# Kernel tuning notes

Measured on AMD Instinct MI355X. Metric: run time of the kernel, lower is better.

## Reference

```python
import jax, jax.numpy as jnp
import numpy as np

N_NODES = 50000
N_EDGES = 1600000
D = 128  # input_dim == hidden_dim


def glorot(key, shape):
    lim = float(np.sqrt(6.0 / (shape[0] + shape[1])))
    return jax.random.uniform(key, shape, jnp.float32, -lim, lim)


def setup_inputs() -> dict:
    key = jax.random.key(0)
    ks = jax.random.split(key, 10)
    x = jax.random.normal(ks[0], (N_NODES, D), jnp.float32)
    edge_index = jax.random.randint(ks[1], (2, N_EDGES), 0, N_NODES, jnp.int64)
    edge_attr = jax.random.normal(ks[2], (N_EDGES, D), jnp.float32)
    # SAGEConv params per layer: lin_l (W,b), lin_r (W, no bias)
    W1l = glorot(ks[3], (D, D)); b1l = jnp.zeros((D,), jnp.float32)
    W1r = glorot(ks[4], (D, D))
    W2l = glorot(ks[5], (D, D)); b2l = jnp.zeros((D,), jnp.float32)
    W2r = glorot(ks[6], (D, D))
    return {"x": x, "edge_index": edge_index, "edge_attr": edge_attr,
            "W1l": W1l, "b1l": b1l, "W1r": W1r,
            "W2l": W2l, "b2l": b2l, "W2r": W2r}


def sage_layer(z, src, dst, edge_attr, Wl, bl, Wr):
    # message: gather x_j, add edge_attr, relu  -> [E, D]
    msg = jax.nn.relu(z[src] + edge_attr)
    # mean aggregation at destination nodes
    agg = jax.ops.segment_sum(msg, dst, num_segments=N_NODES)
    cnt = jax.ops.segment_sum(jnp.ones((dst.shape[0], 1), z.dtype), dst,
                              num_segments=N_NODES)
    agg = agg / jnp.maximum(cnt, 1.0)
    # lin_l(agg) + lin_r(x) (root weight, no bias on lin_r)
    return agg @ Wl + bl + z @ Wr


def reference(x, edge_index, edge_attr, W1l, b1l, W1r, W2l, b2l, W2r):
    src, dst = edge_index[0], edge_index[1]
    z = sage_layer(x, src, dst, edge_attr, W1l, b1l, W1r)
    z = jax.nn.relu(z)  # activation between layers; dropout=0, normalize='none'
    z = sage_layer(z, src, dst, edge_attr, W2l, b2l, W2r)
    return z
```

## Files before the change

kernel.cpp:

```cpp
#include <hip/hip_runtime.h>

#define D 128

typedef __attribute__((ext_vector_type(8))) short bf16x8;
typedef __attribute__((ext_vector_type(4))) float f32x4;
typedef __attribute__((ext_vector_type(4))) unsigned short u16x4;
typedef __attribute__((ext_vector_type(4))) unsigned char u8x4;

__device__ inline unsigned short f2bf(float f) {
    union { float f; unsigned u; } v; v.f = f;
    unsigned r = v.u + 0x7FFF + ((v.u >> 16) & 1);
    return (unsigned short)(r >> 16);
}
__device__ inline float bf2f(unsigned short h) {
    union { unsigned u; float f; } v; v.u = ((unsigned)h) << 16; return v.f;
}
__device__ inline unsigned char f2fp8(float f) {
    unsigned u = __float_as_uint(f);
    unsigned s = (u >> 31) << 7;
    unsigned r = (u & 0x7fffffffu) + 0x7FFFF + ((u >> 20) & 1);
    int e = (int)(r >> 23) - 127;
    if (e < -6) return (unsigned char)s;
    return (unsigned char)(s | ((unsigned)(e + 7) << 3) | ((r >> 20) & 7));
}
__device__ inline float fp82f(unsigned c) {
    unsigned ef = (c >> 3) & 0xF, m = c & 7, s = c >> 7;
    unsigned nb = (s << 31) | ((ef + 120) << 23) | (m << 20);
    float nv = __uint_as_float(nb);
    float sv = (s ? -0.001953125f : 0.001953125f) * (float)m;
    return ef ? nv : sv;
}


__global__ __launch_bounds__(256) void prep_kernel(const float* __restrict__ x,
                                                   unsigned short* __restrict__ xb, int n4,
                                                   const int* __restrict__ dst,
                                                   int* __restrict__ cnt, int E,
                                                   const float* __restrict__ W1l,
                                                   const float* __restrict__ W1r,
                                                   const float* __restrict__ W2l,
                                                   const float* __restrict__ W2r,
                                                   unsigned short* __restrict__ Wt1,
                                                   unsigned short* __restrict__ Wt2,
                                                   const float* __restrict__ ea,
                                                   unsigned char* __restrict__ eaq, int nea4,
                                                   int CAST_B, int CNT_B, int EAQ_B) {
    int b = blockIdx.x, tid = threadIdx.x;
    if (b < CAST_B) {
        int i = b * 256 + tid;
        if (i < n4) {
            float4 v = reinterpret_cast<const float4*>(x)[i];
            ushort4 r;
            r.x = f2bf(v.x); r.y = f2bf(v.y); r.z = f2bf(v.z); r.w = f2bf(v.w);
            reinterpret_cast<ushort4*>(xb)[i] = r;
        }
    } else if (b < CAST_B + CNT_B) {
        int e = (b - CAST_B) * 256 + tid;
        if (e < E) atomicAdd(&cnt[dst[e]], 1);
    } else if (b < CAST_B + CNT_B + 128) {
        int c = b - CAST_B - CNT_B;
        int k = tid;
        float v1 = (k < 128) ? W1l[k * 128 + c] : W1r[(k - 128) * 128 + c];
        float v2 = (k < 128) ? W2l[k * 128 + c] : W2r[(k - 128) * 128 + c];
        Wt1[c * 256 + k] = f2bf(v1);
        Wt2[c * 256 + k] = f2bf(v2);
    } else {
        int i0 = (b - CAST_B - CNT_B - 128) * 256 + tid;
        int step = EAQ_B * 256;
        for (int i = i0; i < nea4; i += step) {
            f32x4 v = __builtin_nontemporal_load(
                reinterpret_cast<const f32x4*>(ea) + i);
            u8x4 q;
            q[0] = f2fp8(v[0]); q[1] = f2fp8(v[1]);
            q[2] = f2fp8(v[2]); q[3] = f2fp8(v[3]);
            reinterpret_cast<u8x4*>(eaq)[i] = q;
        }
    }
}


__global__ __launch_bounds__(256) void psum_kernel(const int* __restrict__ cnt,
                                                   int* __restrict__ bsum, int n) {
    __shared__ int wsh[4];
    int b = blockIdx.x, tid = threadIdx.x;
    int i0 = b * 1024 + tid * 4;
    int s = 0;
    #pragma unroll
    for (int j = 0; j < 4; ++j) { int i = i0 + j; if (i < n) s += cnt[i]; }
    #pragma unroll
    for (int d = 1; d < 64; d <<= 1) s += __shfl_xor(s, d, 64);
    if ((tid & 63) == 0) wsh[tid >> 6] = s;
    __syncthreads();
    if (tid == 0) bsum[b] = wsh[0] + wsh[1] + wsh[2] + wsh[3];
}

__global__ __launch_bounds__(256) void fscan_kernel(const int* __restrict__ cnt,
                                                    const int* __restrict__ bsum,
                                                    int* __restrict__ off,
                                                    int* __restrict__ cursor, int n) {
    __shared__ int wsum[4];
    int b = blockIdx.x, tid = threadIdx.x;
    int lane = tid & 63, wv = tid >> 6;
    int bp = 0;
    for (int j = 0; j < b; ++j) bp += bsum[j];
    int i0 = b * 1024 + tid * 4;
    int v[4]; int s = 0;
    #pragma unroll
    for (int j = 0; j < 4; ++j) { int i = i0 + j; v[j] = (i < n) ? cnt[i] : 0; s += v[j]; }
    int sc = s;
    #pragma unroll
    for (int d = 1; d < 64; d <<= 1) { int u = __shfl_up(sc, d, 64); if (lane >= d) sc += u; }
    if (lane == 63) wsum[wv] = sc;
    __syncthreads();
    int wp = 0;
    for (int j = 0; j < wv; ++j) wp += wsum[j];
    int base = bp + wp + sc - s;
    #pragma unroll
    for (int j = 0; j < 4; ++j) {
        int i = i0 + j;
        if (i < n) { cursor[i] = base; off[i + 1] = base + v[j]; }
        base += v[j];
    }
    if (b == 0 && tid == 0) off[0] = 0;
}


__global__ __launch_bounds__(256) void fill_kernel(const int* __restrict__ src,
                                                   const int* __restrict__ dst,
                                                   int* __restrict__ cursor,
                                                   long long* __restrict__ pairs, int E) {
    int e = blockIdx.x * 256 + threadIdx.x;
    if (e < E) {
        int d = dst[e];
        int slot = atomicAdd(&cursor[d], 1);
        pairs[slot] = (long long)(unsigned)src[e] | ((long long)e << 32);
    }
}


__global__ __launch_bounds__(256) void aggregate_kernel(const unsigned short* __restrict__ featb,
                                                        const unsigned char* __restrict__ eaq,
                                                        const int* __restrict__ off,
                                                        const long long* __restrict__ pairs,
                                                        unsigned short* __restrict__ aggb,
                                                        int N) {
    int nd = blockIdx.x * 4 + (threadIdx.x >> 6);
    if (nd >= N) return;
    int t = threadIdx.x & 63;
    int half = t >> 5, l32 = t & 31;
    int s = off[nd], e = off[nd + 1];
    float a0 = 0.f, a1 = 0.f, a2 = 0.f, a3 = 0.f;

    for (int b = s; b < e; b += 64) {
        int cnt = min(64, e - b);
        long long prl = (b + t < e) ? pairs[b + t] : 0LL;
        int psrc = (int)prl;
        int peid = (int)(prl >> 32);

        auto fetch = [&](int idx, f32x4& ev, u16x4& xv) {
            int sidx = __shfl(psrc, idx, 64);
            int eidx = __shfl(peid, idx, 64);
            u8x4 eq = *reinterpret_cast<const u8x4*>(&eaq[(size_t)eidx * D + l32 * 4]);
            ev[0] = fp82f(eq[0]); ev[1] = fp82f(eq[1]);
            ev[2] = fp82f(eq[2]); ev[3] = fp82f(eq[3]);
            xv = *reinterpret_cast<const u16x4*>(&featb[(size_t)sidx * D + l32 * 4]);
        };
        auto accum = [&](const f32x4& ev, const u16x4& xv) {
            a0 += fmaxf(bf2f(xv[0]) + ev[0], 0.f);
            a1 += fmaxf(bf2f(xv[1]) + ev[1], 0.f);
            a2 += fmaxf(bf2f(xv[2]) + ev[2], 0.f);
            a3 += fmaxf(bf2f(xv[3]) + ev[3], 0.f);
        };

        int p = 0;
        for (; p + 8 <= cnt; p += 8) {
            f32x4 e0, e1, e2, e3; u16x4 x0, x1, x2, x3;
            fetch(p + half, e0, x0);
            fetch(p + 2 + half, e1, x1);
            fetch(p + 4 + half, e2, x2);
            fetch(p + 6 + half, e3, x3);
            accum(e0, x0); accum(e1, x1); accum(e2, x2); accum(e3, x3);
        }
        if (p + 4 <= cnt) {
            f32x4 e0, e1; u16x4 x0, x1;
            fetch(p + half, e0, x0);
            fetch(p + 2 + half, e1, x1);
            accum(e0, x0); accum(e1, x1);
            p += 4;
        }
        if (p + 2 <= cnt) {
            f32x4 e0; u16x4 x0;
            fetch(p + half, e0, x0);
            accum(e0, x0);
            p += 2;
        }
        if (p < cnt) {
            f32x4 e0; u16x4 x0;
            fetch(p, e0, x0);
            if (half == 0) accum(e0, x0);
        }
    }

    a0 += __shfl_xor(a0, 32, 64);
    a1 += __shfl_xor(a1, 32, 64);
    a2 += __shfl_xor(a2, 32, 64);
    a3 += __shfl_xor(a3, 32, 64);
    int deg = e - s;
    float inv = 1.f / (float)(deg > 0 ? deg : 1);
    if (half == 0) {
        u16x4 r;
        r[0] = f2bf(a0 * inv); r[1] = f2bf(a1 * inv);
        r[2] = f2bf(a2 * inv); r[3] = f2bf(a3 * inv);
        *reinterpret_cast<u16x4*>(&aggb[(size_t)nd * D + l32 * 4]) = r;
    }
}


template <int RELU, int OUT_BF16>
__global__ __launch_bounds__(256) void gemm_mfma_kernel(const unsigned short* __restrict__ A1,
                                                        const unsigned short* __restrict__ A2,
                                                        const unsigned short* __restrict__ Wt,
                                                        const float* __restrict__ bias,
                                                        float* __restrict__ outf,
                                                        unsigned short* __restrict__ outb,
                                                        int MT, int N) {
    int tid = threadIdx.x;
    int w = tid >> 6;
    int l = tid & 63;
    int lr = l & 15;
    int lg = l >> 4;
    int c0 = w * 32;

    bf16x8 bfr[2][8];
    #pragma unroll
    for (int t = 0; t < 2; ++t)
        #pragma unroll
        for (int kc = 0; kc < 8; ++kc)
            bfr[t][kc] = *reinterpret_cast<const bf16x8*>(
                &Wt[(size_t)(c0 + t * 16 + lr) * 256 + kc * 32 + lg * 8]);

    for (int mt = blockIdx.x; mt < MT; mt += gridDim.x) {
        int r0 = mt * 32;
        f32x4 acc[2][2];
        #pragma unroll
        for (int tr = 0; tr < 2; ++tr)
            #pragma unroll
            for (int tc = 0; tc < 2; ++tc) acc[tr][tc] = {0.f, 0.f, 0.f, 0.f};

        #pragma unroll
        for (int kc = 0; kc < 8; ++kc) {
            const unsigned short* Ap = (kc < 4) ? A1 : A2;
            int k = (kc & 3) * 32 + lg * 8;
            bf16x8 af0 = *reinterpret_cast<const bf16x8*>(&Ap[(size_t)(r0 + lr) * D + k]);
            bf16x8 af1 = *reinterpret_cast<const bf16x8*>(&Ap[(size_t)(r0 + 16 + lr) * D + k]);
            acc[0][0] = __builtin_amdgcn_mfma_f32_16x16x32_bf16(af0, bfr[0][kc], acc[0][0], 0, 0, 0);
            acc[1][0] = __builtin_amdgcn_mfma_f32_16x16x32_bf16(af1, bfr[0][kc], acc[1][0], 0, 0, 0);
            acc[0][1] = __builtin_amdgcn_mfma_f32_16x16x32_bf16(af0, bfr[1][kc], acc[0][1], 0, 0, 0);
            acc[1][1] = __builtin_amdgcn_mfma_f32_16x16x32_bf16(af1, bfr[1][kc], acc[1][1], 0, 0, 0);
        }

        #pragma unroll
        for (int tc = 0; tc < 2; ++tc) {
            int col = c0 + tc * 16 + lr;
            float bv = bias[col];
            #pragma unroll
            for (int tr = 0; tr < 2; ++tr) {
                #pragma unroll
                for (int r = 0; r < 4; ++r) {
                    int row = r0 + tr * 16 + lg * 4 + r;
                    if (row < N) {
                        float v = acc[tr][tc][r] + bv;
                        if (RELU) v = fmaxf(v, 0.f);
                        if (OUT_BF16) outb[(size_t)row * D + col] = f2bf(v);
                        else outf[(size_t)row * D + col] = v;
                    }
                }
            }
        }
    }
}

extern "C" void kernel_launch(void* const* d_in, const int* in_sizes, int n_in,
                              void* d_out, int out_size, void* d_ws, size_t ws_size,
                              hipStream_t stream) {
    const float* x   = (const float*)d_in[0];
    const int*   ei  = (const int*)d_in[1];
    const float* ea  = (const float*)d_in[2];
    const float* W1l = (const float*)d_in[3];
    const float* b1l = (const float*)d_in[4];
    const float* W1r = (const float*)d_in[5];
    const float* W2l = (const float*)d_in[6];
    const float* b2l = (const float*)d_in[7];
    const float* W2r = (const float*)d_in[8];
    float* out = (float*)d_out;

    const int N = in_sizes[0] / D;
    const int E = in_sizes[1] / 2;
    const int NP = (N + 31) & ~31;
    const int* src = ei;
    const int* dst = ei + E;

    char* ws = (char*)d_ws;
    size_t o = 0;
    auto alloc = [&](size_t bytes) -> void* {
        void* p = ws + o;
        o = (o + bytes + 255) & ~(size_t)255;
        return p;
    };
    int*   cnt    = (int*)alloc((size_t)N * 4);
    int*   off    = (int*)alloc((size_t)(N + 1) * 4);
    int*   cursor = (int*)alloc((size_t)N * 4);
    int*   bsum   = (int*)alloc(256 * 4);
    long long* pairs = (long long*)alloc((size_t)E * 8);
    unsigned char* eaq = (unsigned char*)alloc((size_t)E * D);
    unsigned short* xb   = (unsigned short*)alloc((size_t)NP * D * 2);
    unsigned short* z1b  = (unsigned short*)alloc((size_t)NP * D * 2);
    unsigned short* aggb = (unsigned short*)alloc((size_t)NP * D * 2);
    unsigned short* Wt1  = (unsigned short*)alloc(128 * 256 * 2);
    unsigned short* Wt2  = (unsigned short*)alloc(128 * 256 * 2);
    (void)ws_size; (void)n_in; (void)out_size;

    const int MT = (N + 31) / 32;
    const int NB = (N + 1023) / 1024;
    const int AGB = (N + 3) / 4;
    const int n4 = N * D / 4;
    const int nea4 = (int)((size_t)E * D / 4);
    const int CAST_B = (n4 + 255) / 256;
    const int CNT_B = (E + 255) / 256;
    const int EAQ_B = 8192;

    (void)hipMemsetAsync(cnt, 0, (size_t)N * 4, stream);
    prep_kernel<<<CAST_B + CNT_B + 128 + EAQ_B, 256, 0, stream>>>(
        x, xb, n4, dst, cnt, E, W1l, W1r, W2l, W2r, Wt1, Wt2,
        ea, eaq, nea4, CAST_B, CNT_B, EAQ_B);
    psum_kernel<<<NB, 256, 0, stream>>>(cnt, bsum, N);
    fscan_kernel<<<NB, 256, 0, stream>>>(cnt, bsum, off, cursor, N);
    fill_kernel<<<(E + 255) / 256, 256, 0, stream>>>(src, dst, cursor, pairs, E);

    aggregate_kernel<<<AGB, 256, 0, stream>>>(xb, eaq, off, pairs, aggb, N);
    gemm_mfma_kernel<1, 1><<<1024, 256, 0, stream>>>(aggb, xb, Wt1, b1l, nullptr, z1b, MT, N);

    aggregate_kernel<<<AGB, 256, 0, stream>>>(z1b, eaq, off, pairs, aggb, N);
    gemm_mfma_kernel<0, 0><<<1024, 256, 0, stream>>>(aggb, z1b, Wt2, b2l, out, nullptr, MT, N);
}
```

Baseline: 679.1 us.

## Fuse all stages into one cooperative persistent kernel and drop fp8 edge attributes

Replaces the sequence of prep, scan, fill, aggregate and GEMM launches with a single cooperative kernel that runs each stage in turn, separated by grid-wide syncs and using grid-stride loops. It also stops quantizing edge_attr to fp8 and instead reads the fp32 edge attributes directly, with nontemporal loads, in both aggregation passes. The GEMM template parameters become runtime arguments. This removes launch gaps and the separate quantization pass over the 800MB edge_attr tensor, but each aggregation now reads four times as many edge-attribute bytes. The grid is also capped at 256×(up to 4) blocks, which may reduce latency hiding in the gather-heavy phases.

```diff
diff --git a/kernel.cpp b/kernel.cpp
--- a/kernel.cpp
+++ b/kernel.cpp
@@ -1,11 +1,13 @@
 #include <hip/hip_runtime.h>
+#include <hip/hip_cooperative_groups.h>
+
+namespace cg = cooperative_groups;
 
 #define D 128
 
 typedef __attribute__((ext_vector_type(8))) short bf16x8;
 typedef __attribute__((ext_vector_type(4))) float f32x4;
 typedef __attribute__((ext_vector_type(4))) unsigned short u16x4;
-typedef __attribute__((ext_vector_type(4))) unsigned char u8x4;
 
 __device__ inline unsigned short f2bf(float f) {
     union { float f; unsigned u; } v; v.f = f;
@@ -15,215 +17,94 @@
 __device__ inline float bf2f(unsigned short h) {
     union { unsigned u; float f; } v; v.u = ((unsigned)h) << 16; return v.f;
 }
-__device__ inline unsigned char f2fp8(float f) {
-    unsigned u = __float_as_uint(f);
-    unsigned s = (u >> 31) << 7;
-    unsigned r = (u & 0x7fffffffu) + 0x7FFFF + ((u >> 20) & 1);
-    int e = (int)(r >> 23) - 127;
-    if (e < -6) return (unsigned char)s;
-    return (unsigned char)(s | ((unsigned)(e + 7) << 3) | ((r >> 20) & 7));
-}
-__device__ inline float fp82f(unsigned c) {
-    unsigned ef = (c >> 3) & 0xF, m = c & 7, s = c >> 7;
-    unsigned nb = (s << 31) | ((ef + 120) << 23) | (m << 20);
-    float nv = __uint_as_float(nb);
-    float sv = (s ? -0.001953125f : 0.001953125f) * (float)m;
-    return ef ? nv : sv;
-}
-
-
-__global__ __launch_bounds__(256) void prep_kernel(const float* __restrict__ x,
-                                                   unsigned short* __restrict__ xb, int n4,
-                                                   const int* __restrict__ dst,
-                                                   int* __restrict__ cnt, int E,
-                                                   const float* __restrict__ W1l,
-                                                   const float* __restrict__ W1r,
-                                                   const float* __restrict__ W2l,
-                                                   const float* __restrict__ W2r,
-                                                   unsigned short* __restrict__ Wt1,
-                                                   unsigned short* __restrict__ Wt2,
-                                                   const float* __restrict__ ea,
-                                                   unsigned char* __restrict__ eaq, int nea4,
-                                                   int CAST_B, int CNT_B, int EAQ_B) {
-    int b = blockIdx.x, tid = threadIdx.x;
-    if (b < CAST_B) {
-        int i = b * 256 + tid;
-        if (i < n4) {
-            float4 v = reinterpret_cast<const float4*>(x)[i];
-            ushort4 r;
-            r.x = f2bf(v.x); r.y = f2bf(v.y); r.z = f2bf(v.z); r.w = f2bf(v.w);
-            reinterpret_cast<ushort4*>(xb)[i] = r;
-        }
-    } else if (b < CAST_B + CNT_B) {
-        int e = (b - CAST_B) * 256 + tid;
-        if (e < E) atomicAdd(&cnt[dst[e]], 1);
-    } else if (b < CAST_B + CNT_B + 128) {
-        int c = b - CAST_B - CNT_B;
-        int k = tid;
-        float v1 = (k < 128) ? W1l[k * 128 + c] : W1r[(k - 128) * 128 + c];
-        float v2 = (k < 128) ? W2l[k * 128 + c] : W2r[(k - 128) * 128 + c];
-        Wt1[c * 256 + k] = f2bf(v1);
-        Wt2[c * 256 + k] = f2bf(v2);
-    } else {
-        int i0 = (b - CAST_B - CNT_B - 128) * 256 + tid;
-        int step = EAQ_B * 256;
-        for (int i = i0; i < nea4; i += step) {
-            f32x4 v = __builtin_nontemporal_load(
-                reinterpret_cast<const f32x4*>(ea) + i);
-            u8x4 q;
-            q[0] = f2fp8(v[0]); q[1] = f2fp8(v[1]);
-            q[2] = f2fp8(v[2]); q[3] = f2fp8(v[3]);
-            reinterpret_cast<u8x4*>(eaq)[i] = q;
-        }
-    }
-}
-
-
-__global__ __launch_bounds__(256) void psum_kernel(const int* __restrict__ cnt,
-                                                   int* __restrict__ bsum, int n) {
-    __shared__ int wsh[4];
-    int b = blockIdx.x, tid = threadIdx.x;
-    int i0 = b * 1024 + tid * 4;
-    int s = 0;
-    #pragma unroll
-    for (int j = 0; j < 4; ++j) { int i = i0 + j; if (i < n) s += cnt[i]; }
-    #pragma unroll
-    for (int d = 1; d < 64; d <<= 1) s += __shfl_xor(s, d, 64);
-    if ((tid & 63) == 0) wsh[tid >> 6] = s;
-    __syncthreads();
-    if (tid == 0) bsum[b] = wsh[0] + wsh[1] + wsh[2] + wsh[3];
-}
-
-__global__ __launch_bounds__(256) void fscan_kernel(const int* __restrict__ cnt,
-                                                    const int* __restrict__ bsum,
-                                                    int* __restrict__ off,
-                                                    int* __restrict__ cursor, int n) {
-    __shared__ int wsum[4];
-    int b = blockIdx.x, tid = threadIdx.x;
-    int lane = tid & 63, wv = tid >> 6;
-    int bp = 0;
-    for (int j = 0; j < b; ++j) bp += bsum[j];
-    int i0 = b * 1024 + tid * 4;
-    int v[4]; int s = 0;
-    #pragma unroll
-    for (int j = 0; j < 4; ++j) { int i = i0 + j; v[j] = (i < n) ? cnt[i] : 0; s += v[j]; }
-    int sc = s;
-    #pragma unroll
-    for (int d = 1; d < 64; d <<= 1) { int u = __shfl_up(sc, d, 64); if (lane >= d) sc += u; }
-    if (lane == 63) wsum[wv] = sc;
-    __syncthreads();
-    int wp = 0;
-    for (int j = 0; j < wv; ++j) wp += wsum[j];
-    int base = bp + wp + sc - s;
-    #pragma unroll
-    for (int j = 0; j < 4; ++j) {
-        int i = i0 + j;
-        if (i < n) { cursor[i] = base; off[i + 1] = base + v[j]; }
-        base += v[j];
-    }
-    if (b == 0 && tid == 0) off[0] = 0;
-}
-
-
-__global__ __launch_bounds__(256) void fill_kernel(const int* __restrict__ src,
-                                                   const int* __restrict__ dst,
-                                                   int* __restrict__ cursor,
-                                                   long long* __restrict__ pairs, int E) {
-    int e = blockIdx.x * 256 + threadIdx.x;
-    if (e < E) {
-        int d = dst[e];
-        int slot = atomicAdd(&cursor[d], 1);
-        pairs[slot] = (long long)(unsigned)src[e] | ((long long)e << 32);
-    }
-}
-
-
-__global__ __launch_bounds__(256) void aggregate_kernel(const unsigned short* __restrict__ featb,
-                                                        const unsigned char* __restrict__ eaq,
-                                                        const int* __restrict__ off,
-                                                        const long long* __restrict__ pairs,
-                                                        unsigned short* __restrict__ aggb,
-                                                        int N) {
-    int nd = blockIdx.x * 4 + (threadIdx.x >> 6);
-    if (nd >= N) return;
+
+
+__device__ void agg_phase(const unsigned short* __restrict__ featb,
+                          const float* __restrict__ ea,
+                          const int* __restrict__ off,
+                          const long long* __restrict__ pairs,
+                          unsigned short* __restrict__ aggb, int N) {
     int t = threadIdx.x & 63;
     int half = t >> 5, l32 = t & 31;
-    int s = off[nd], e = off[nd + 1];
-    float a0 = 0.f, a1 = 0.f, a2 = 0.f, a3 = 0.f;
-
-    for (int b = s; b < e; b += 64) {
-        int cnt = min(64, e - b);
-        long long prl = (b + t < e) ? pairs[b + t] : 0LL;
-        int psrc = (int)prl;
-        int peid = (int)(prl >> 32);
-
-        auto fetch = [&](int idx, f32x4& ev, u16x4& xv) {
-            int sidx = __shfl(psrc, idx, 64);
-            int eidx = __shfl(peid, idx, 64);
-            u8x4 eq = *reinterpret_cast<const u8x4*>(&eaq[(size_t)eidx * D + l32 * 4]);
-            ev[0] = fp82f(eq[0]); ev[1] = fp82f(eq[1]);
-            ev[2] = fp82f(eq[2]); ev[3] = fp82f(eq[3]);
-            xv = *reinterpret_cast<const u16x4*>(&featb[(size_t)sidx * D + l32 * 4]);
-        };
-        auto accum = [&](const f32x4& ev, const u16x4& xv) {
-            a0 += fmaxf(bf2f(xv[0]) + ev[0], 0.f);
-            a1 += fmaxf(bf2f(xv[1]) + ev[1], 0.f);
-            a2 += fmaxf(bf2f(xv[2]) + ev[2], 0.f);
-            a3 += fmaxf(bf2f(xv[3]) + ev[3], 0.f);
-        };
-
-        int p = 0;
-        for (; p + 8 <= cnt; p += 8) {
-            f32x4 e0, e1, e2, e3; u16x4 x0, x1, x2, x3;
-            fetch(p + half, e0, x0);
-            fetch(p + 2 + half, e1, x1);
-            fetch(p + 4 + half, e2, x2);
-            fetch(p + 6 + half, e3, x3);
-            accum(e0, x0); accum(e1, x1); accum(e2, x2); accum(e3, x3);
-        }
-        if (p + 4 <= cnt) {
-            f32x4 e0, e1; u16x4 x0, x1;
-            fetch(p + half, e0, x0);
-            fetch(p + 2 + half, e1, x1);
-            accum(e0, x0); accum(e1, x1);
-            p += 4;
-        }
-        if (p + 2 <= cnt) {
-            f32x4 e0; u16x4 x0;
-            fetch(p + half, e0, x0);
-            accum(e0, x0);
-            p += 2;
-        }
-        if (p < cnt) {
-            f32x4 e0; u16x4 x0;
-            fetch(p, e0, x0);
-            if (half == 0) accum(e0, x0);
-        }
-    }
-
-    a0 += __shfl_xor(a0, 32, 64);
-    a1 += __shfl_xor(a1, 32, 64);
-    a2 += __shfl_xor(a2, 32, 64);
-    a3 += __shfl_xor(a3, 32, 64);
-    int deg = e - s;
-    float inv = 1.f / (float)(deg > 0 ? deg : 1);
-    if (half == 0) {
-        u16x4 r;
-        r[0] = f2bf(a0 * inv); r[1] = f2bf(a1 * inv);
-        r[2] = f2bf(a2 * inv); r[3] = f2bf(a3 * inv);
-        *reinterpret_cast<u16x4*>(&aggb[(size_t)nd * D + l32 * 4]) = r;
-    }
-}
-
-
-template <int RELU, int OUT_BF16>
-__global__ __launch_bounds__(256) void gemm_mfma_kernel(const unsigned short* __restrict__ A1,
-                                                        const unsigned short* __restrict__ A2,
-                                                        const unsigned short* __restrict__ Wt,
-                                                        const float* __restrict__ bias,
-                                                        float* __restrict__ outf,
-                                                        unsigned short* __restrict__ outb,
-                                                        int MT, int N) {
+    int gw = (blockIdx.x * 256 + threadIdx.x) >> 6;
+    int TW = (gridDim.x * 256) >> 6;
+
+    for (int nd = gw; nd < N; nd += TW) {
+        int s = off[nd], e = off[nd + 1];
+        float a0 = 0.f, a1 = 0.f, a2 = 0.f, a3 = 0.f;
+
+        for (int b = s; b < e; b += 64) {
+            int cnt = min(64, e - b);
+            long long prl = (b + t < e) ? __builtin_nontemporal_load(&pairs[b + t]) : 0LL;
+            int psrc = (int)prl;
+            int peid = (int)(prl >> 32);
+
+            auto fetch = [&](int idx, f32x4& ev, u16x4& xv) {
+                int sidx = __shfl(psrc, idx, 64);
+                int eidx = __shfl(peid, idx, 64);
+                ev = __builtin_nontemporal_load(
+                    reinterpret_cast<const f32x4*>(&ea[(size_t)eidx * D + l32 * 4]));
+                xv = *reinterpret_cast<const u16x4*>(&featb[(size_t)sidx * D + l32 * 4]);
+            };
+            auto accum = [&](const f32x4& ev, const u16x4& xv) {
+                a0 += fmaxf(bf2f(xv[0]) + ev[0], 0.f);
+                a1 += fmaxf(bf2f(xv[1]) + ev[1], 0.f);
+                a2 += fmaxf(bf2f(xv[2]) + ev[2], 0.f);
+                a3 += fmaxf(bf2f(xv[3]) + ev[3], 0.f);
+            };
+
+            int p = 0;
+            for (; p + 8 <= cnt; p += 8) {
+                f32x4 e0, e1, e2, e3; u16x4 x0, x1, x2, x3;
+                fetch(p + half, e0, x0);
+                fetch(p + 2 + half, e1, x1);
+                fetch(p + 4 + half, e2, x2);
+                fetch(p + 6 + half, e3, x3);
+                accum(e0, x0); accum(e1, x1); accum(e2, x2); accum(e3, x3);
+            }
+            if (p + 4 <= cnt) {
+                f32x4 e0, e1; u16x4 x0, x1;
+                fetch(p + half, e0, x0);
+                fetch(p + 2 + half, e1, x1);
+                accum(e0, x0); accum(e1, x1);
+                p += 4;
+            }
+            if (p + 2 <= cnt) {
+                f32x4 e0; u16x4 x0;
+                fetch(p + half, e0, x0);
+                accum(e0, x0);
+                p += 2;
+            }
+            if (p < cnt) {
+                f32x4 e0; u16x4 x0;
+                fetch(p, e0, x0);
+                if (half == 0) accum(e0, x0);
+            }
+        }
+
+        a0 += __shfl_xor(a0, 32, 64);
+        a1 += __shfl_xor(a1, 32, 64);
+        a2 += __shfl_xor(a2, 32, 64);
+        a3 += __shfl_xor(a3, 32, 64);
+        int deg = e - s;
+        float inv = 1.f / (float)(deg > 0 ? deg : 1);
+        if (half == 0) {
+            u16x4 r;
+            r[0] = f2bf(a0 * inv); r[1] = f2bf(a1 * inv);
+            r[2] = f2bf(a2 * inv); r[3] = f2bf(a3 * inv);
+            *reinterpret_cast<u16x4*>(&aggb[(size_t)nd * D + l32 * 4]) = r;
+        }
+    }
+}
+
+
+__device__ void gemm_phase(const unsigned short* __restrict__ A1,
+                           const unsigned short* __restrict__ A2,
+                           const unsigned short* __restrict__ Wt,
+                           const float* __restrict__ bias,
+                           float* __restrict__ outf,
+                           unsigned short* __restrict__ outb,
+                           int MT, int N, int RELU, int OBF) {
     int tid = threadIdx.x;
     int w = tid >> 6;
     int l = tid & 63;
@@ -271,13 +152,109 @@
                     if (row < N) {
                         float v = acc[tr][tc][r] + bv;
                         if (RELU) v = fmaxf(v, 0.f);
-                        if (OUT_BF16) outb[(size_t)row * D + col] = f2bf(v);
+                        if (OBF) outb[(size_t)row * D + col] = f2bf(v);
                         else outf[(size_t)row * D + col] = v;
                     }
                 }
             }
         }
     }
+}
+
+
+__global__ __launch_bounds__(256, 4) void mega_kernel(
+    const float* __restrict__ x, const int* __restrict__ src,
+    const int* __restrict__ dst, const float* __restrict__ ea,
+    const float* __restrict__ W1l, const float* __restrict__ b1l,
+    const float* __restrict__ W1r, const float* __restrict__ W2l,
+    const float* __restrict__ b2l, const float* __restrict__ W2r,
+    int* __restrict__ cnt, int* __restrict__ bsum, int* __restrict__ off,
+    int* __restrict__ cursor, long long* __restrict__ pairs,
+    unsigned short* __restrict__ xb, unsigned short* __restrict__ z1b,
+    unsigned short* __restrict__ aggb,
+    unsigned short* __restrict__ Wt1, unsigned short* __restrict__ Wt2,
+    float* __restrict__ out, int N, int E, int NB, int MT) {
+    cg::grid_group g = cg::this_grid();
+    __shared__ int wsh[4];
+    int tid = threadIdx.x;
+    int gtid = blockIdx.x * 256 + tid;
+    int gsz = gridDim.x * 256;
+
+    int n4 = N * D / 4;
+    for (int i = gtid; i < n4; i += gsz) {
+        float4 v = reinterpret_cast<const float4*>(x)[i];
+        ushort4 r;
+        r.x = f2bf(v.x); r.y = f2bf(v.y); r.z = f2bf(v.z); r.w = f2bf(v.w);
+        reinterpret_cast<ushort4*>(xb)[i] = r;
+    }
+    for (int e = gtid; e < E; e += gsz) atomicAdd(&cnt[dst[e]], 1);
+    for (int i = gtid; i < 128 * 256; i += gsz) {
+        int c = i >> 8, k = i & 255;
+        float v1 = (k < 128) ? W1l[k * 128 + c] : W1r[(k - 128) * 128 + c];
+        float v2 = (k < 128) ? W2l[k * 128 + c] : W2r[(k - 128) * 128 + c];
+        Wt1[c * 256 + k] = f2bf(v1);
+        Wt2[c * 256 + k] = f2bf(v2);
+    }
+    g.sync();
+
+    for (int b = blockIdx.x; b < NB; b += gridDim.x) {
+        int i0 = b * 1024 + tid * 4;
+        int s = 0;
+        #pragma unroll
+        for (int j = 0; j < 4; ++j) { int i = i0 + j; if (i < N) s += cnt[i]; }
+        #pragma unroll
+        for (int d = 1; d < 64; d <<= 1) s += __shfl_xor(s, d, 64);
+        if ((tid & 63) == 0) wsh[tid >> 6] = s;
+        __syncthreads();
+        if (tid == 0) bsum[b] = wsh[0] + wsh[1] + wsh[2] + wsh[3];
+        __syncthreads();
+    }
+    g.sync();
+
+    for (int b = blockIdx.x; b < NB; b += gridDim.x) {
+        int lane = tid & 63, wv = tid >> 6;
+        int bp = 0;
+        for (int j = 0; j < b; ++j) bp += bsum[j];
+        int i0 = b * 1024 + tid * 4;
+        int v[4]; int s = 0;
+        #pragma unroll
+        for (int j = 0; j < 4; ++j) { int i = i0 + j; v[j] = (i < N) ? cnt[i] : 0; s += v[j]; }
+        int sc = s;
+        #pragma unroll
+        for (int d = 1; d < 64; d <<= 1) { int u = __shfl_up(sc, d, 64); if (lane >= d) sc += u; }
+        if (lane == 63) wsh[wv] = sc;
+        __syncthreads();
+        int wp = 0;
+        for (int j = 0; j < wv; ++j) wp += wsh[j];
+        int base = bp + wp + sc - s;
+        #pragma unroll
+        for (int j = 0; j < 4; ++j) {
+            int i = i0 + j;
+            if (i < N) { cursor[i] = base; off[i + 1] = base + v[j]; }
+            base += v[j];
+        }
+        if (b == 0 && tid == 0) off[0] = 0;
+        __syncthreads();
+    }
+    g.sync();
+
+    for (int e = gtid; e < E; e += gsz) {
+        int d2 = dst[e];
+        int slot = atomicAdd(&cursor[d2], 1);
+        pairs[slot] = (long long)(unsigned)src[e] | ((long long)e << 32);
+    }
+    g.sync();
+
+    agg_phase(xb, ea, off, pairs, aggb, N);
+    g.sync();
+
+    gemm_phase(aggb, xb, Wt1, b1l, nullptr, z1b, MT, N, 1, 1);
+    g.sync();
+
+    agg_phase(z1b, ea, off, pairs, aggb, N);
+    g.sync();
+
+    gemm_phase(aggb, z1b, Wt2, b2l, out, nullptr, MT, N, 0, 0);
 }
 
 extern "C" void kernel_launch(void* const* d_in, const int* in_sizes, int n_in,
@@ -312,7 +289,6 @@
     int*   cursor = (int*)alloc((size_t)N * 4);
     int*   bsum   = (int*)alloc(256 * 4);
     long long* pairs = (long long*)alloc((size_t)E * 8);
-    unsigned char* eaq = (unsigned char*)alloc((size_t)E * D);
     unsigned short* xb   = (unsigned short*)alloc((size_t)NP * D * 2);
     unsigned short* z1b  = (unsigned short*)alloc((size_t)NP * D * 2);
     unsigned short* aggb = (unsigned short*)alloc((size_t)NP * D * 2);
@@ -320,26 +296,24 @@
     unsigned short* Wt2  = (unsigned short*)alloc(128 * 256 * 2);
     (void)ws_size; (void)n_in; (void)out_size;
 
-    const int MT = (N + 31) / 32;
-    const int NB = (N + 1023) / 1024;
-    const int AGB = (N + 3) / 4;
-    const int n4 = N * D / 4;
-    const int nea4 = (int)((size_t)E * D / 4);
-    const int CAST_B = (n4 + 255) / 256;
-    const int CNT_B = (E + 255) / 256;
-    const int EAQ_B = 8192;
+    int NB = (N + 1023) / 1024;
+    int MT = (N + 31) / 32;
 
     (void)hipMemsetAsync(cnt, 0, (size_t)N * 4, stream);
-    prep_kernel<<<CAST_B + CNT_B + 128 + EAQ_B, 256, 0, stream>>>(
-        x, xb, n4, dst, cnt, E, W1l, W1r, W2l, W2r, Wt1, Wt2,
-        ea, eaq, nea4, CAST_B, CNT_B, EAQ_B);
-    psum_kernel<<<NB, 256, 0, stream>>>(cnt, bsum, N);
-    fscan_kernel<<<NB, 256, 0, stream>>>(cnt, bsum, off, cursor, N);
-    fill_kernel<<<(E + 255) / 256, 256, 0, stream>>>(src, dst, cursor, pairs, E);
-
-    aggregate_kernel<<<AGB, 256, 0, stream>>>(xb, eaq, off, pairs, aggb, N);
-    gemm_mfma_kernel<1, 1><<<1024, 256, 0, stream>>>(aggb, xb, Wt1, b1l, nullptr, z1b, MT, N);
-
-    aggregate_kernel<<<AGB, 256, 0, stream>>>(z1b, eaq, off, pairs, aggb, N);
-    gemm_mfma_kernel<0, 0><<<1024, 256, 0, stream>>>(aggb, z1b, Wt2, b2l, out, nullptr, MT, N);
-}
+
+    int maxB = 0;
+    (void)hipOccupancyMaxActiveBlocksPerMultiprocessor(&maxB, mega_kernel, 256, 0);
+    if (maxB < 1) maxB = 1;
+    if (maxB > 4) maxB = 4;
+    int GB = maxB * 256;
+
+    void* args[] = {
+        (void*)&x, (void*)&src, (void*)&dst, (void*)&ea,
+        (void*)&W1l, (void*)&b1l, (void*)&W1r,
+        (void*)&W2l, (void*)&b2l, (void*)&W2r,
+        (void*)&cnt, (void*)&bsum, (void*)&off, (void*)&cursor, (void*)&pairs,
+        (void*)&xb, (void*)&z1b, (void*)&aggb, (void*)&Wt1, (void*)&Wt2,
+        (void*)&out, (void*)&N, (void*)&E, (void*)&NB, (void*)&MT
+    };
+    (void)hipLaunchCooperativeKernel(mega_kernel, dim3(GB), dim3(256), args, 0, stream);
+}
```

New measurement: 1.044 ms. 1.54x slower.
